# Optimization experiments

Measured on AMD Instinct MI355X. Metric: run time of the kernel, lower is better.

## Reference

```python
import jax, jax.numpy as jnp
import numpy as np

SAI, B, CK, H, W = 9, 4, 64, 32, 32
CV = 64
RADIUS = 4.0 / 8.0  # valid_dis_range / 8


def setup_inputs() -> dict:
    key = jax.random.key(0)
    k1, k2, k3, k4, k5 = jax.random.split(key, 5)
    return {
        "memory_keys": jax.random.normal(k1, (SAI, B, CK, H, W), dtype=jnp.float32),
        "memory_values": jax.random.normal(k2, (SAI, B, CV, H, W), dtype=jnp.float32),
        "query_query": jax.random.normal(k3, (B, CK, H, W), dtype=jnp.float32),
        "disparity": jax.random.normal(k4, (B, 1, H, W), dtype=jnp.float32),
        "sequence_index": jax.random.randint(k5, (B, SAI, 2), 0, 11, dtype=jnp.int32),
    }


def reference(memory_keys, memory_values, query_query, disparity, sequence_index):
    sai, b, ck, h, w = memory_keys.shape
    cv = memory_values.shape[2]
    shw = sai * h * w

    # keys: (sai,b,ck,h,w) -> (b, ck, sai*h*w)
    keys = jnp.transpose(memory_keys, (1, 2, 0, 3, 4)).reshape(b, ck, shw)
    # query: (b, ck, h*w) -> (b, h*w, ck)
    q = query_query.reshape(b, ck, h * w).transpose(0, 2, 1)
    # scores: (b, h*w, sai*h*w)
    scores = jnp.einsum("bqc,bck->bqk", q, keys)

    # distance-based additive mask (per batch, per frame, per key pixel)
    seq = sequence_index.astype(jnp.float32)
    dist = jnp.sqrt((seq[:, :, 1] - 5.0) ** 2 + (seq[:, :, 0] - 5.0) ** 2)  # (b, sai)
    # total_disparity: (b, sai, h, w); disparity is (b,1,h,w)
    total = dist[:, :, None, None] * disparity
    large = jnp.abs(total) > RADIUS  # mask==1 where |disp| exceeds radius
    # bias: 0 where mask==1, -inf where mask==0 (per original masked_fill)
    bias = jnp.where(large, 0.0, -jnp.inf).reshape(b, 1, shw)

    scores = scores + bias  # broadcasts over query positions
    attn = jax.nn.softmax(scores, axis=-1)

    # values: (sai,b,cv,h,w) -> (b, sai*h*w, cv)
    vals = jnp.transpose(memory_values, (1, 2, 0, 3, 4)).reshape(b, cv, shw).transpose(0, 2, 1)
    mem = jnp.einsum("bqk,bkc->bqc", attn, vals)  # (b, h*w, cv)
    return mem.transpose(0, 2, 1).reshape(b, cv, h, w)
```

## Files before the change

### kernel.cpp

```cpp
#include <hip/hip_runtime.h>
#include <math.h>

#define SAI 9
#define NB  4
#define CK  64
#define CV  64
#define HW  1024
#define QT  32
#define RSW 136
#define RSTR 68

typedef __attribute__((ext_vector_type(8))) short bf16x8;
typedef __attribute__((ext_vector_type(4))) float f32x4;
typedef unsigned short u16;
typedef unsigned int u32;

__device__ __forceinline__ u16 f2bf(float x) {
    unsigned u = __float_as_uint(x);
    return (u16)((u + 0x7fff + ((u >> 16) & 1)) >> 16);
}
__device__ __forceinline__ float bf2f(u16 s) {
    return __uint_as_float(((unsigned)s) << 16);
}
__device__ __forceinline__ unsigned pk2(float a, float b) {
    return (unsigned)f2bf(a) | ((unsigned)f2bf(b) << 16);
}
__device__ __forceinline__ void lds_barrier() {
    __asm__ __volatile__("s_waitcnt lgkmcnt(0)\n\ts_barrier" ::: "memory");
}

__global__ __launch_bounds__(256) void cfa_prep(
    const float* __restrict__ keys, const float* __restrict__ vals,
    u16* __restrict__ khi, u16* __restrict__ klo, u16* __restrict__ vbf)
{
    const int gid = blockIdx.x * 256 + threadIdx.x;
    const int isV = gid >= (SAI * NB * 8192);
    const int id  = isV ? gid - SAI * NB * 8192 : gid;
    const int f   = id >> 13;
    const int r   = id & 8191;
    const int lane = r & 63;
    const int gg   = r >> 6;
    const int l15 = lane & 15, quad = lane >> 4;
    const size_t fb = (size_t)f * (64 * 1024);

    if (!isV) {
        const int p  = (gg >> 1) * 16 + l15;
        const int c0 = (gg & 1) * 32 + quad * 8;
        const float* src = keys + fb + (size_t)c0 * HW + p;
        float x[8];
#pragma unroll
        for (int j = 0; j < 8; ++j) x[j] = src[(size_t)j * HW];
        uint4 ph, pl;
        u32* php = (u32*)&ph; u32* plp = (u32*)&pl;
#pragma unroll
        for (int h2 = 0; h2 < 4; ++h2) {
            u16 h0 = f2bf(x[h2 * 2]),     h1 = f2bf(x[h2 * 2 + 1]);
            u16 l0 = f2bf(x[h2 * 2] - bf2f(h0));
            u16 l1 = f2bf(x[h2 * 2 + 1] - bf2f(h1));
            php[h2] = (u32)h0 | ((u32)h1 << 16);
            plp[h2] = (u32)l0 | ((u32)l1 << 16);
        }
        const size_t dst = fb + (size_t)gg * 512 + lane * 8;
        *(uint4*)&khi[dst] = ph;
        *(uint4*)&klo[dst] = pl;
    } else {
        const int p = (gg >> 2) * 32 + quad * 8;
        const int c = (gg & 3) * 16 + l15;
        const float* src = vals + fb + (size_t)c * HW + p;
        const float4 a = *(const float4*)src;
        const float4 b = *(const float4*)(src + 4);
        uint4 pv;
        pv.x = pk2(a.x, a.y); pv.y = pk2(a.z, a.w);
        pv.z = pk2(b.x, b.y); pv.w = pk2(b.z, b.w);
        *(uint4*)&vbf[fb + (size_t)gg * 512 + lane * 8] = pv;
    }
}

__global__ __launch_bounds__(256, 3) void cfa_main(
    const u16* __restrict__ khi, const u16* __restrict__ klo,
    const u16* __restrict__ vbf,
    const float* __restrict__ query, const float* __restrict__ disp,
    const int* __restrict__ seq,
    float* __restrict__ numW, float* __restrict__ denW)
{
    __shared__ alignas(16) u16 sW[2][QT * RSW];
    __shared__ float sDen[4 * QT];

    const int tid = threadIdx.x;
    const int w = tid >> 6;
    const int lane = tid & 63;
    const int l15 = lane & 15, quad = lane >> 4;
    const int b  = blockIdx.y;
    const int s  = blockIdx.z;
    const int p0 = blockIdx.x * QT;
    const int f  = s * NB + b;
    const size_t fb = (size_t)f * (64 * 1024);

    const float d0 = (float)seq[(b * SAI + s) * 2 + 0] - 5.f;
    const float d1 = (float)seq[(b * SAI + s) * 2 + 1] - 5.f;
    const float dist = sqrtf(d0 * d0 + d1 * d1);

    bf16x8 qh[2][2], ql[2][2];
#pragma unroll
    for (int q2 = 0; q2 < 2; ++q2)
#pragma unroll
        for (int ks = 0; ks < 2; ++ks)
#pragma unroll
            for (int j = 0; j < 8; ++j) {
                float x = query[(size_t)(b * CK + ks * 32 + quad * 8 + j) * HW + p0 + q2 * 16 + l15];
                u16 h = f2bf(x);
                qh[q2][ks][j] = (short)h;
                ql[q2][ks][j] = (short)f2bf(x - bf2f(h));
            }

    f32x4 acc[2];
#pragma unroll
    for (int q2 = 0; q2 < 2; ++q2)
#pragma unroll
        for (int r = 0; r < 4; ++r) acc[q2][r] = 0.f;
    float den[2] = {0.f, 0.f};

    uint4 kbh[2][2], kbl[2][2];
#define LOADK(tt)                                                              \
    {                                                                          \
        _Pragma("unroll") for (int kt = 0; kt < 2; ++kt)                       \
        _Pragma("unroll") for (int ks = 0; ks < 2; ++ks) {                     \
            const size_t ka = fb +                                             \
                (size_t)((((tt) * 8 + w * 2 + kt) * 2) + ks) * 512 + lane * 8; \
            kbh[kt][ks] = *(const uint4*)&khi[ka];                             \
            kbl[kt][ks] = *(const uint4*)&klo[ka];                             \
        }                                                                      \
    }

    LOADK(0);

    for (int t = 0; t < 8; ++t) {
        u16* const wbuf = sW[t & 1];

        uint4 vb[4];
#pragma unroll
        for (int k2 = 0; k2 < 4; ++k2)
            vb[k2] = *(const uint4*)&vbf[fb + (size_t)((t * 4 + k2) * 4 + w) * 512 + lane * 8];
        const float4 dv0 = *(const float4*)(disp + b * HW + t * 128 + w * 32 + quad * 4);
        const float4 dv1 = *(const float4*)(disp + b * HW + t * 128 + w * 32 + 16 + quad * 4);

        f32x4 sc[2][2];
#pragma unroll
        for (int q2 = 0; q2 < 2; ++q2)
#pragma unroll
            for (int kt = 0; kt < 2; ++kt)
#pragma unroll
                for (int r = 0; r < 4; ++r) sc[q2][kt][r] = 0.f;

#pragma unroll
        for (int kt = 0; kt < 2; ++kt)
#pragma unroll
            for (int ks = 0; ks < 2; ++ks) {
                const bf16x8 kh = __builtin_bit_cast(bf16x8, kbh[kt][ks]);
                const bf16x8 kl = __builtin_bit_cast(bf16x8, kbl[kt][ks]);
#pragma unroll
                for (int q2 = 0; q2 < 2; ++q2) {
                    sc[q2][kt] = __builtin_amdgcn_mfma_f32_16x16x32_bf16(kh, qh[q2][ks], sc[q2][kt], 0, 0, 0);
                    sc[q2][kt] = __builtin_amdgcn_mfma_f32_16x16x32_bf16(kl, qh[q2][ks], sc[q2][kt], 0, 0, 0);
                    sc[q2][kt] = __builtin_amdgcn_mfma_f32_16x16x32_bf16(kh, ql[q2][ks], sc[q2][kt], 0, 0, 0);
                }
            }

#pragma unroll
        for (int kt = 0; kt < 2; ++kt) {
            const float4 dv = kt ? dv1 : dv0;
            const float m0 = (fabsf(dist * dv.x) > 0.5f) ? 1.f : 0.f;
            const float m1 = (fabsf(dist * dv.y) > 0.5f) ? 1.f : 0.f;
            const float m2 = (fabsf(dist * dv.z) > 0.5f) ? 1.f : 0.f;
            const float m3 = (fabsf(dist * dv.w) > 0.5f) ? 1.f : 0.f;
#pragma unroll
            for (int q2 = 0; q2 < 2; ++q2) {
                const float e0 = m0 * __expf(sc[q2][kt][0]);
                const float e1 = m1 * __expf(sc[q2][kt][1]);
                const float e2 = m2 * __expf(sc[q2][kt][2]);
                const float e3 = m3 * __expf(sc[q2][kt][3]);
                den[q2] += (e0 + e1) + (e2 + e3);
                uint2 pk;
                pk.x = pk2(e0, e1);
                pk.y = pk2(e2, e3);
                *(uint2*)&wbuf[(q2 * 16 + l15) * RSW + w * 32 + kt * 16 + quad * 4] = pk;
            }
        }

        LOADK((t + 1) & 7);

        lds_barrier();

#pragma unroll
        for (int k2 = 0; k2 < 4; ++k2) {
            const bf16x8 vf = __builtin_bit_cast(bf16x8, vb[k2]);
#pragma unroll
            for (int q2 = 0; q2 < 2; ++q2) {
                const bf16x8 wf = __builtin_bit_cast(bf16x8,
                    *(const uint4*)&wbuf[(q2 * 16 + l15) * RSW + k2 * 32 + quad * 8]);
                acc[q2] = __builtin_amdgcn_mfma_f32_16x16x32_bf16(wf, vf, acc[q2], 0, 0, 0);
            }
        }
    }
#undef LOADK

#pragma unroll
    for (int q2 = 0; q2 < 2; ++q2) {
        den[q2] += __shfl_xor(den[q2], 16, 64);
        den[q2] += __shfl_xor(den[q2], 32, 64);
    }
    if (quad == 0) {
#pragma unroll
        for (int q2 = 0; q2 < 2; ++q2)
            sDen[w * QT + q2 * 16 + l15] = den[q2];
    }
    __syncthreads();
    if (tid < QT)
        denW[(size_t)f * HW + p0 + tid] =
            sDen[tid] + sDen[QT + tid] + sDen[2 * QT + tid] + sDen[3 * QT + tid];

#pragma unroll
    for (int q2 = 0; q2 < 2; ++q2)
#pragma unroll
        for (int r = 0; r < 4; ++r) {
            const int q = q2 * 16 + quad * 4 + r;
            const int c = w * 16 + l15;
            numW[((size_t)f * HW + p0 + q) * CV + c] = acc[q2][r];
        }
}

__global__ __launch_bounds__(256) void cfa_reduce(
    const float* __restrict__ numW, const float* __restrict__ denW,
    float* __restrict__ out)
{
    const int tid = threadIdx.x;
    const int bid = blockIdx.x;
    const int b = bid >> 8;
    const int p = (bid & 255) * 4 + (tid >> 6);
    const int c = tid & 63;
    float num = 0.f, den = 0.f;
#pragma unroll
    for (int s = 0; s < SAI; ++s) {
        num += numW[(((size_t)(s * NB + b)) * HW + p) * CV + c];
        den += denW[((size_t)(s * NB + b)) * HW + p];
    }
    out[((size_t)b * CV + c) * HW + p] = num / den;
}

__global__ __launch_bounds__(256, 2) void cfa_fb(
    const float* __restrict__ keys, const float* __restrict__ vals,
    const float* __restrict__ query, const float* __restrict__ disp,
    const int* __restrict__ seq,
    float* __restrict__ numW, float* __restrict__ denW,
    float* __restrict__ out, int nS)
{
    __shared__ alignas(16) unsigned int sV[CV * RSTR];
    __shared__ alignas(16) unsigned int sWb[32 * RSTR];
    __shared__ float sDen[4 * 32];
    __shared__ float sDenTot[32];

    const int tid  = threadIdx.x;
    const int w    = tid >> 6;
    const int lane = tid & 63;
    const int l15  = lane & 15;
    const int quad = lane >> 4;
    const int b    = blockIdx.y;
    const int s0   = blockIdx.z;
    const int p0   = blockIdx.x * 32;
    const bool direct = (nS == SAI);

    bf16x8 qhi[2][2], qlo[2][2];
#pragma unroll
    for (int qt = 0; qt < 2; ++qt)
#pragma unroll
        for (int ks = 0; ks < 2; ++ks)
#pragma unroll
            for (int j = 0; j < 8; ++j) {
                float x = query[(size_t)(b * CK + ks * 32 + quad * 8 + j) * HW + p0 + qt * 16 + l15];
                u16 h = f2bf(x);
                qhi[qt][ks][j] = (short)h;
                qlo[qt][ks][j] = (short)f2bf(x - bf2f(h));
            }

    f32x4 acc[2];
#pragma unroll
    for (int qt = 0; qt < 2; ++qt)
#pragma unroll
        for (int r = 0; r < 4; ++r) acc[qt][r] = 0.f;
    float denacc[2][4] = {{0.f,0.f,0.f,0.f},{0.f,0.f,0.f,0.f}};

    for (int si = 0; si < nS; ++si) {
        const int s = s0 + si;
        const float d0 = (float)seq[(b * SAI + s) * 2 + 0] - 5.f;
        const float d1 = (float)seq[(b * SAI + s) * 2 + 1] - 5.f;
        const float dist = sqrtf(d0 * d0 + d1 * d1);
        const float* Kf = keys + (size_t)(s * NB + b) * CK * HW;
        const float* Vf = vals + (size_t)(s * NB + b) * CV * HW;

        for (int t = 0; t < HW / 128; ++t) {
            const int t128 = t * 128;
            __syncthreads();
#pragma unroll
            for (int it = 0; it < 4; ++it) {
                const int gidx = it * 256 + tid;
                const int c = gidx >> 4;
                const int g = gidx & 15;
                const float* vp = Vf + (size_t)c * HW + t128 + g * 8;
                const float4 f0 = *(const float4*)(vp);
                const float4 f1 = *(const float4*)(vp + 4);
                uint4 pk;
                pk.x = pk2(f0.x, f0.y); pk.y = pk2(f0.z, f0.w);
                pk.z = pk2(f1.x, f1.y); pk.w = pk2(f1.z, f1.w);
                *(uint4*)&sV[c * RSTR + g * 4] = pk;
            }

            f32x4 sc[2][2];
#pragma unroll
            for (int qt = 0; qt < 2; ++qt)
#pragma unroll
                for (int kt = 0; kt < 2; ++kt)
#pragma unroll
                    for (int r = 0; r < 4; ++r) sc[qt][kt][r] = 0.f;

            const int keyBase = t128 + w * 32 + l15;
#pragma unroll
            for (int kt = 0; kt < 2; ++kt)
#pragma unroll
                for (int ks = 0; ks < 2; ++ks) {
                    bf16x8 kh, kl;
#pragma unroll
                    for (int j = 0; j < 8; ++j) {
                        float x = Kf[(size_t)(ks * 32 + quad * 8 + j) * HW + keyBase + kt * 16];
                        u16 h = f2bf(x);
                        kh[j] = (short)h;
                        kl[j] = (short)f2bf(x - bf2f(h));
                    }
#pragma unroll
                    for (int qt = 0; qt < 2; ++qt) {
                        sc[qt][kt] = __builtin_amdgcn_mfma_f32_16x16x32_bf16(qhi[qt][ks], kh, sc[qt][kt], 0, 0, 0);
                        sc[qt][kt] = __builtin_amdgcn_mfma_f32_16x16x32_bf16(qhi[qt][ks], kl, sc[qt][kt], 0, 0, 0);
                        sc[qt][kt] = __builtin_amdgcn_mfma_f32_16x16x32_bf16(qlo[qt][ks], kh, sc[qt][kt], 0, 0, 0);
                    }
                }

#pragma unroll
            for (int kt = 0; kt < 2; ++kt) {
                const int kk = w * 32 + kt * 16 + l15;
                const float dvv = disp[b * HW + t128 + kk];
                const float msk = (fabsf(dist * dvv) > 0.5f) ? 1.f : 0.f;
#pragma unroll
                for (int qt = 0; qt < 2; ++qt)
#pragma unroll
                    for (int r = 0; r < 4; ++r) {
                        const float e = msk * __expf(sc[qt][kt][r]);
                        denacc[qt][r] += e;
                        const int q = qt * 16 + quad * 4 + r;
                        ((u16*)sWb)[q * (2 * RSTR) + kk] = f2bf(e);
                    }
            }
            __syncthreads();

            const int c = w * 16 + l15;
#pragma unroll
            for (int ks2 = 0; ks2 < 4; ++ks2) {
                const int g = ks2 * 4 + quad;
                uint4 vr = *(uint4*)&sV[c * RSTR + g * 4];
                bf16x8 vfrag = __builtin_bit_cast(bf16x8, vr);
#pragma unroll
                for (int qt = 0; qt < 2; ++qt) {
                    const int q = qt * 16 + l15;
                    uint4 wr = *(uint4*)&sWb[q * RSTR + g * 4];
                    bf16x8 wfrag = __builtin_bit_cast(bf16x8, wr);
                    acc[qt] = __builtin_amdgcn_mfma_f32_16x16x32_bf16(wfrag, vfrag, acc[qt], 0, 0, 0);
                }
            }
        }
    }

#pragma unroll
    for (int off = 1; off < 16; off <<= 1)
#pragma unroll
        for (int qt = 0; qt < 2; ++qt)
#pragma unroll
            for (int r = 0; r < 4; ++r)
                denacc[qt][r] += __shfl_xor(denacc[qt][r], off, 64);

    if (l15 == 0)
#pragma unroll
        for (int qt = 0; qt < 2; ++qt)
#pragma unroll
            for (int r = 0; r < 4; ++r)
                sDen[w * 32 + qt * 16 + quad * 4 + r] = denacc[qt][r];
    __syncthreads();

    if (tid < 32) {
        const float d = sDen[tid] + sDen[32 + tid] + sDen[64 + tid] + sDen[96 + tid];
        if (direct) sDenTot[tid] = d;
        else        denW[(size_t)(s0 * NB + b) * HW + p0 + tid] = d;
    }

    if (direct) {
        __syncthreads();
#pragma unroll
        for (int qt = 0; qt < 2; ++qt)
#pragma unroll
            for (int r = 0; r < 4; ++r) {
                const int q = qt * 16 + quad * 4 + r;
                const int c = w * 16 + l15;
                out[((size_t)b * CV + c) * HW + p0 + q] = acc[qt][r] / sDenTot[q];
            }
    } else {
#pragma unroll
        for (int qt = 0; qt < 2; ++qt)
#pragma unroll
            for (int r = 0; r < 4; ++r) {
                const int q = qt * 16 + quad * 4 + r;
                const int c = w * 16 + l15;
                numW[((size_t)(s0 * NB + b) * HW + p0 + q) * CV + c] = acc[qt][r];
            }
    }
}

extern "C" void kernel_launch(void* const* d_in, const int* in_sizes, int n_in,
                              void* d_out, int out_size, void* d_ws, size_t ws_size,
                              hipStream_t stream) {
    const float* keys  = (const float*)d_in[0];
    const float* vals  = (const float*)d_in[1];
    const float* query = (const float*)d_in[2];
    const float* disp  = (const float*)d_in[3];
    const int*   seq   = (const int*)d_in[4];
    float* out = (float*)d_out;

    const size_t numElems = (size_t)SAI * NB * HW * CV;
    const size_t denElems = (size_t)SAI * NB * HW;
    const size_t partBytes = (numElems + denElems) * sizeof(float);
    const size_t fragBytes = (size_t)SAI * NB * CK * HW * 2;
    const size_t needFull = partBytes + 3 * fragBytes;

    float* numW = (float*)d_ws;
    float* denW = numW + numElems;

    if (ws_size >= needFull) {
        u16* khi = (u16*)((char*)d_ws + partBytes);
        u16* klo = (u16*)((char*)khi + fragBytes);
        u16* vbf = (u16*)((char*)klo + fragBytes);
        hipLaunchKernelGGL(cfa_prep, dim3(2 * SAI * NB * 8192 / 256), dim3(256), 0, stream,
                           keys, vals, khi, klo, vbf);
        hipLaunchKernelGGL(cfa_main, dim3(HW / QT, NB, SAI), dim3(256), 0, stream,
                           khi, klo, vbf, query, disp, seq, numW, denW);
        hipLaunchKernelGGL(cfa_reduce, dim3(1024), dim3(256), 0, stream,
                           numW, denW, out);
    } else if (ws_size >= partBytes) {
        hipLaunchKernelGGL(cfa_fb, dim3(HW / 32, NB, SAI), dim3(256), 0, stream,
                           keys, vals, query, disp, seq, numW, denW, (float*)nullptr, 1);
        hipLaunchKernelGGL(cfa_reduce, dim3(1024), dim3(256), 0, stream,
                           numW, denW, out);
    } else {
        hipLaunchKernelGGL(cfa_fb, dim3(HW / 32, NB, 1), dim3(256), 0, stream,
                           keys, vals, query, disp, seq,
                           (float*)nullptr, (float*)nullptr, out, SAI);
    }
}
```

Before: 114.4 us.

## Fuse cross-frame reduction into main kernel via last-block atomic counter

Removes the separate cfa_reduce launch. Each main block bumps a per-tile atomic counter after writing its partials, and the last of the SAI frame blocks sums the numerators and denominators, then writes the normalized output through an LDS transpose. It also moves the next key-tile prefetch ahead of the exp/mask stage to overlap loads with compute. The cost is a memset launch, fences and atomics per block, and a serialized tail reduction done by one block per tile.

```diff
diff --git a/kernel.cpp b/kernel.cpp
--- a/kernel.cpp
+++ b/kernel.cpp
@@ -81,10 +81,12 @@
     const u16* __restrict__ vbf,
     const float* __restrict__ query, const float* __restrict__ disp,
     const int* __restrict__ seq,
-    float* __restrict__ numW, float* __restrict__ denW)
+    float* __restrict__ numW, float* __restrict__ denW,
+    unsigned* __restrict__ cnt, float* __restrict__ out)
 {
     __shared__ alignas(16) u16 sW[2][QT * RSW];
     __shared__ float sDen[4 * QT];
+    __shared__ unsigned sLast;
 
     const int tid = threadIdx.x;
     const int w = tid >> 6;
@@ -166,6 +168,8 @@
                 }
             }
 
+        LOADK((t + 1) & 7);
+
 #pragma unroll
         for (int kt = 0; kt < 2; ++kt) {
             const float4 dv = kt ? dv1 : dv0;
@@ -187,8 +191,6 @@
             }
         }
 
-        LOADK((t + 1) & 7);
-
         lds_barrier();
 
 #pragma unroll
@@ -227,6 +229,51 @@
             const int c = w * 16 + l15;
             numW[((size_t)f * HW + p0 + q) * CV + c] = acc[q2][r];
         }
+
+    __threadfence();
+    __syncthreads();
+    if (tid == 0) {
+        unsigned old = __hip_atomic_fetch_add(&cnt[blockIdx.x * NB + b], 1u,
+                                              __ATOMIC_ACQ_REL,
+                                              __HIP_MEMORY_SCOPE_AGENT);
+        sLast = (old == SAI - 1) ? 1u : 0u;
+    }
+    __syncthreads();
+    if (sLast) {
+        __threadfence();
+        const int q  = tid >> 3;
+        const int c0 = (tid & 7) * 8;
+        float a8[8] = {0.f,0.f,0.f,0.f,0.f,0.f,0.f,0.f};
+        for (int ss = 0; ss < SAI; ++ss) {
+            const float* src = &numW[((size_t)(ss * NB + b) * HW + p0 + q) * CV + c0];
+            const float4 x = *(const float4*)src;
+            const float4 y = *(const float4*)(src + 4);
+            a8[0] += x.x; a8[1] += x.y; a8[2] += x.z; a8[3] += x.w;
+            a8[4] += y.x; a8[5] += y.y; a8[6] += y.z; a8[7] += y.w;
+        }
+        if (tid < QT) {
+            float ds = 0.f;
+            for (int ss = 0; ss < SAI; ++ss)
+                ds += denW[(size_t)(ss * NB + b) * HW + p0 + tid];
+            sDen[tid] = ds;
+        }
+        float* sFin = (float*)sW;
+        __syncthreads();
+#pragma unroll
+        for (int i = 0; i < 8; ++i) sFin[q * 66 + c0 + i] = a8[i];
+        __syncthreads();
+        const int c  = tid >> 2;
+        const int q4 = (tid & 3) * 8;
+        float4 o0, o1;
+#pragma unroll
+        for (int i = 0; i < 4; ++i) {
+            ((float*)&o0)[i] = sFin[(q4 + i) * 66 + c] / sDen[q4 + i];
+            ((float*)&o1)[i] = sFin[(q4 + 4 + i) * 66 + c] / sDen[q4 + 4 + i];
+        }
+        float* dst = &out[((size_t)b * CV + c) * HW + p0 + q4];
+        *(float4*)dst = o0;
+        *(float4*)(dst + 4) = o1;
+    }
 }
 
 __global__ __launch_bounds__(256) void cfa_reduce(
@@ -435,7 +482,8 @@
     const size_t denElems = (size_t)SAI * NB * HW;
     const size_t partBytes = (numElems + denElems) * sizeof(float);
     const size_t fragBytes = (size_t)SAI * NB * CK * HW * 2;
-    const size_t needFull = partBytes + 3 * fragBytes;
+    const size_t cntBytes  = 512;
+    const size_t needFull = partBytes + 3 * fragBytes + cntBytes;
 
     float* numW = (float*)d_ws;
     float* denW = numW + numElems;
@@ -444,12 +492,12 @@
         u16* khi = (u16*)((char*)d_ws + partBytes);
         u16* klo = (u16*)((char*)khi + fragBytes);
         u16* vbf = (u16*)((char*)klo + fragBytes);
+        unsigned* cnt = (unsigned*)((char*)vbf + fragBytes);
+        hipMemsetAsync(cnt, 0, cntBytes, stream);
         hipLaunchKernelGGL(cfa_prep, dim3(2 * SAI * NB * 8192 / 256), dim3(256), 0, stream,
                            keys, vals, khi, klo, vbf);
         hipLaunchKernelGGL(cfa_main, dim3(HW / QT, NB, SAI), dim3(256), 0, stream,
-                           khi, klo, vbf, query, disp, seq, numW, denW);
-        hipLaunchKernelGGL(cfa_reduce, dim3(1024), dim3(256), 0, stream,
-                           numW, denW, out);
+                           khi, klo, vbf, query, disp, seq, numW, denW, cnt, out);
     } else if (ws_size >= partBytes) {
         hipLaunchKernelGGL(cfa_fb, dim3(HW / 32, NB, SAI), dim3(256), 0, stream,
                            keys, vals, query, disp, seq, numW, denW, (float*)nullptr, 1);
```

Result: slower. 275.0 us (+140.4%).
